# Kernel tuning notes

Measured on AMD Instinct MI355X. Metric: run time of the kernel, lower is better.

## Reference

```python
import jax, jax.numpy as jnp
import numpy as np

B, H, W, C = 32, 56, 56, 192
WS, SHIFT, HEADS = 7, 3, 6
HEAD_DIM = C // HEADS
SCALE = 0.17677669529663687  # 1/sqrt(32), passed as qk_scale
HIDDEN = 4 * C
N = WS * WS
EPS = 1e-3


def _rel_index(ws):
    coords = np.stack(np.meshgrid(np.arange(ws), np.arange(ws), indexing='ij')).reshape(2, -1)
    rel = (coords[:, :, None] - coords[:, None, :]).transpose(1, 2, 0)
    rel[:, :, 0] += ws - 1
    rel[:, :, 1] += ws - 1
    rel[:, :, 0] *= 2 * ws - 1
    return rel.sum(-1)  # [N, N] int


def _attn_mask(h, w, ws, ss):
    img = np.zeros((h, w), np.float32)
    cnt = 0
    for hs in (slice(0, -ws), slice(-ws, -ss), slice(-ss, None)):
        for wsl in (slice(0, -ws), slice(-ws, -ss), slice(-ss, None)):
            img[hs, wsl] = cnt
            cnt += 1
    win = img.reshape(h // ws, ws, w // ws, ws).transpose(0, 2, 1, 3).reshape(-1, ws * ws)
    diff = win[:, None, :] - win[:, :, None]
    return np.where(diff != 0, -100.0, 0.0).astype(np.float32)  # [nW, N, N]


REL_IDX = jnp.asarray(_rel_index(WS).reshape(-1))          # [N*N]
ATTN_MASK = jnp.asarray(_attn_mask(H, W, WS, SHIFT))       # [nW, N, N]
NW = ATTN_MASK.shape[0]


def _window_partition(x, ws):
    b, h, w, c = x.shape
    x = x.reshape(b, h // ws, ws, w // ws, ws, c).transpose(0, 1, 3, 2, 4, 5)
    return x.reshape(-1, ws, ws, c)


def _window_reverse(x, ws, h, w):
    c = x.shape[-1]
    x = x.reshape(-1, h // ws, w // ws, ws, ws, c).transpose(0, 1, 3, 2, 4, 5)
    return x.reshape(-1, h, w, c)


def _layer_norm(x, g, b):
    mu = jnp.mean(x, axis=-1, keepdims=True)
    var = jnp.var(x, axis=-1, keepdims=True)
    return (x - mu) * jax.lax.rsqrt(var + EPS) * g + b


def _forward(x, ln1_g, ln1_b, w_qkv, b_qkv, bias_table, w_proj, b_proj,
             ln2_g, ln2_b, w_ffn1, bn1_scale, bn1_shift, w_ffn2, bn2_scale, bn2_shift):
    shortcut = x
    h = _layer_norm(x, ln1_g, ln1_b)
    h = jnp.roll(h, (-SHIFT, -SHIFT), axis=(1, 2))
    xw = _window_partition(h, WS).reshape(-1, N, C)  # [B*nW, N, C]

    qkv = xw @ w_qkv + b_qkv                          # [B*nW, N, 3C]
    qkv = qkv.reshape(-1, N, 3, HEADS, HEAD_DIM).transpose(2, 0, 3, 1, 4)
    q, k, v = qkv[0] * SCALE, qkv[1], qkv[2]          # [B*nW, heads, N, hd]

    attn = jnp.einsum('whnd,whmd->whnm', q, k)        # [B*nW, heads, N, N]
    rel_bias = bias_table[REL_IDX].reshape(N, N, HEADS).transpose(2, 0, 1)
    attn = attn + rel_bias[None]
    attn = attn.reshape(-1, NW, HEADS, N, N) + ATTN_MASK[None, :, None]
    attn = jax.nn.softmax(attn.reshape(-1, HEADS, N, N), axis=-1)

    o = jnp.einsum('whnm,whmd->whnd', attn, v)        # [B*nW, heads, N, hd]
    o = o.transpose(0, 2, 1, 3).reshape(-1, N, C)
    o = o @ w_proj + b_proj

    o = _window_reverse(o.reshape(-1, WS, WS, C), WS, H, W)
    o = jnp.roll(o, (SHIFT, SHIFT), axis=(1, 2))
    x = shortcut + o

    y = _layer_norm(x, ln2_g, ln2_b)
    dn = ('NHWC', 'HWIO', 'NHWC')
    y = jax.lax.conv_general_dilated(y, w_ffn1, (1, 1), 'SAME', dimension_numbers=dn)
    y = y * bn1_scale + bn1_shift
    y = jax.nn.gelu(y, approximate=False)
    y = jax.lax.conv_general_dilated(y, w_ffn2, (1, 1), 'SAME', dimension_numbers=dn)
    y = y * bn2_scale + bn2_shift
    return x + y


def setup_inputs() -> dict:
    key = jax.random.key(0)
    ks = jax.random.split(key, 8)
    s = lambda n: 0.02
    return {
        'x': jax.random.normal(ks[0], (B, H, W, C), jnp.float32),
        'ln1_g': jnp.ones((C,), jnp.float32),
        'ln1_b': jnp.zeros((C,), jnp.float32),
        'w_qkv': jax.random.normal(ks[1], (C, 3 * C), jnp.float32) * (C ** -0.5),
        'b_qkv': jnp.zeros((3 * C,), jnp.float32),
        'bias_table': jax.random.truncated_normal(ks[2], -2.0, 2.0, ((2 * WS - 1) ** 2, HEADS), jnp.float32) * 0.02,
        'w_proj': jax.random.normal(ks[3], (C, C), jnp.float32) * (C ** -0.5),
        'b_proj': jnp.zeros((C,), jnp.float32),
        'ln2_g': jnp.ones((C,), jnp.float32),
        'ln2_b': jnp.zeros((C,), jnp.float32),
        'w_ffn1': jax.random.normal(ks[4], (3, 3, C, HIDDEN), jnp.float32) * ((9 * C) ** -0.5),
        'bn1_scale': jnp.ones((HIDDEN,), jnp.float32),
        'bn1_shift': jnp.zeros((HIDDEN,), jnp.float32),
        'w_ffn2': jax.random.normal(ks[5], (1, 1, HIDDEN, C), jnp.float32) * (HIDDEN ** -0.5),
        'bn2_scale': jnp.ones((C,), jnp.float32),
        'bn2_shift': jnp.zeros((C,), jnp.float32),
    }


def reference(x, ln1_g, ln1_b, w_qkv, b_qkv, bias_table, w_proj, b_proj,
              ln2_g, ln2_b, w_ffn1, bn1_scale, bn1_shift, w_ffn2, bn2_scale, bn2_shift):
    return _forward(x, ln1_g, ln1_b, w_qkv, b_qkv, bias_table, w_proj, b_proj,
                    ln2_g, ln2_b, w_ffn1, bn1_scale, bn1_shift, w_ffn2, bn2_scale, bn2_shift)
```

## Files before the change

### kernel.cpp

```cpp
#include <hip/hip_runtime.h>
#include <hip/hip_bf16.h>
#include <math.h>

#define DEVINL __device__ __forceinline__

typedef __bf16 bf16x8 __attribute__((ext_vector_type(8)));
typedef float  f32x4  __attribute__((ext_vector_type(4)));
typedef unsigned int u32x4 __attribute__((ext_vector_type(4)));

DEVINL float bf2f(unsigned short h){ return __builtin_bit_cast(float, (unsigned)h << 16); }
DEVINL unsigned short f2bf(float f){
  unsigned u = __builtin_bit_cast(unsigned, f);
  u += 0x7fffu + ((u >> 16) & 1u);
  return (unsigned short)(u >> 16);
}

DEVINL void gl16(const unsigned short* g, unsigned short* l){
  __builtin_amdgcn_global_load_lds((const __attribute__((address_space(1))) unsigned int*)g,
                                   (__attribute__((address_space(3))) unsigned int*)l,
                                   16, 0, 0);
}

DEVINL unsigned ldsoff(const void* p){
  return (unsigned)(unsigned long long)(const __attribute__((address_space(3))) char*)p;
}
DEVINL bf16x8 dsr16(const unsigned short* p){
  u32x4 r;
  asm volatile("ds_read_b128 %0, %1" : "=v"(r) : "v"(ldsoff(p)));
  return __builtin_bit_cast(bf16x8, r);
}

#define Bn 32
#define Hn 56
#define Wn 56
#define Cn 192
#define WSz 7
#define SHIFTn 3
#define HEADSn 6
#define HDn 32
#define NWIN 49
#define NPIX (Bn*Hn*Wn)
#define HIDDENn 768
#define KCONV (9*Cn)
#define PADH 58
#define QKSCALE 0.17677669529663687f

DEVINL float wave_sum(float v){
  #pragma unroll
  for (int off=32; off; off>>=1) v += __shfl_xor(v, off, 64);
  return v;
}

__global__ __launch_bounds__(256) void k_ln1(const float* __restrict__ x,
                                             const float* __restrict__ g,
                                             const float* __restrict__ bb,
                                             unsigned short* __restrict__ h)
{
  int row  = blockIdx.x*4 + (threadIdx.x >> 6);
  int lane = threadIdx.x & 63;
  int win = row / NWIN, n = row % NWIN;
  int b = win >> 6, rem = win & 63, wh = rem >> 3, ww = rem & 7;
  int i = n / WSz, j = n % WSz;
  int rr = (wh*WSz + i + SHIFTn) % Hn;
  int cc = (ww*WSz + j + SHIFTn) % Wn;
  const float* xr = x + (size_t)((b*Hn + rr)*Wn + cc)*Cn;
  float v0 = xr[lane], v1 = xr[lane+64], v2 = xr[lane+128];
  float s  = wave_sum(v0+v1+v2);
  float sq = wave_sum(v0*v0+v1*v1+v2*v2);
  float mu = s * (1.0f/Cn);
  float var = sq * (1.0f/Cn) - mu*mu;
  float rs = rsqrtf(var + 1e-3f);
  unsigned short* hr = h + (size_t)row*Cn;
  hr[lane]     = f2bf((v0-mu)*rs*g[lane]     + bb[lane]);
  hr[lane+64]  = f2bf((v1-mu)*rs*g[lane+64]  + bb[lane+64]);
  hr[lane+128] = f2bf((v2-mu)*rs*g[lane+128] + bb[lane+128]);
}

__global__ __launch_bounds__(256) void k_ln2(const float* __restrict__ xmid,
                                             const float* __restrict__ g,
                                             const float* __restrict__ bb,
                                             unsigned short* __restrict__ out)
{
  int p    = blockIdx.x*4 + (threadIdx.x >> 6);
  int lane = threadIdx.x & 63;
  int b = p / (Hn*Wn), rc = p % (Hn*Wn);
  int r = rc / Wn, c = rc % Wn;
  const float* xr = xmid + (size_t)p*Cn;
  float v0 = xr[lane], v1 = xr[lane+64], v2 = xr[lane+128];
  float s  = wave_sum(v0+v1+v2);
  float sq = wave_sum(v0*v0+v1*v1+v2*v2);
  float mu = s * (1.0f/Cn);
  float var = sq * (1.0f/Cn) - mu*mu;
  float rs = rsqrtf(var + 1e-3f);
  unsigned short* orow = out + (size_t)((b*PADH + r + 1)*PADH + (c + 1))*Cn;
  orow[lane]     = f2bf((v0-mu)*rs*g[lane]     + bb[lane]);
  orow[lane+64]  = f2bf((v1-mu)*rs*g[lane+64]  + bb[lane+64]);
  orow[lane+128] = f2bf((v2-mu)*rs*g[lane+128] + bb[lane+128]);
}

__global__ __launch_bounds__(256) void k_transpose(const float* __restrict__ in,
                                                   unsigned short* __restrict__ out,
                                                   int K, int N)
{
  int idx = blockIdx.x*256 + threadIdx.x;
  if (idx < K*N){ int k = idx / N, n = idx - k*N; out[(size_t)n*K + k] = f2bf(in[idx]); }
}

__global__ __launch_bounds__(256) void k_attn(const unsigned short* __restrict__ qkv,
                                              const float* __restrict__ bias_table,
                                              unsigned short* __restrict__ o,
                                              int win_base)
{
  __shared__ float qs[NWIN][HDn], ks[NWIN][HDn], vs[NWIN][HDn], S[NWIN][NWIN+1];
  int head = blockIdx.x, lwin = blockIdx.y;
  int gwin = win_base + lwin;
  int tid = threadIdx.x;
  const unsigned short* base = qkv + (size_t)lwin*NWIN*576 + head*HDn;
  for (int t = tid; t < NWIN*HDn; t += 256){
    int n = t >> 5, d = t & 31;
    const unsigned short* rp = base + (size_t)n*576 + d;
    qs[n][d] = bf2f(rp[0]) * QKSCALE;
    ks[n][d] = bf2f(rp[192]);
    vs[n][d] = bf2f(rp[384]);
  }
  __syncthreads();
  int rem = gwin & 63, wh = rem >> 3, ww = rem & 7;
  for (int t = tid; t < NWIN*NWIN; t += 256){
    int p = t / NWIN, q = t - p*NWIN;
    float acc = 0.f;
    #pragma unroll
    for (int d = 0; d < HDn; ++d) acc += qs[p][d]*ks[q][d];
    int pi = p/7, pj = p%7, qi = q/7, qj = q%7;
    int rel = (pi-qi+6)*13 + (pj-qj+6);
    acc += bias_table[rel*HEADSn + head];
    int pr = wh*7+pi, pc = ww*7+pj, qr = wh*7+qi, qc = ww*7+qj;
    int cp = (pr<49?0:(pr<53?1:2))*3 + (pc<49?0:(pc<53?1:2));
    int cq = (qr<49?0:(qr<53?1:2))*3 + (qc<49?0:(qc<53?1:2));
    if (cp != cq) acc -= 100.0f;
    S[p][q] = acc;
  }
  __syncthreads();
  if (tid < NWIN){
    float m = -1e30f;
    for (int q=0;q<NWIN;++q) m = fmaxf(m, S[tid][q]);
    float sum = 0.f;
    for (int q=0;q<NWIN;++q){ float e = expf(S[tid][q]-m); S[tid][q]=e; sum+=e; }
    float inv = 1.0f/sum;
    for (int q=0;q<NWIN;++q) S[tid][q] *= inv;
  }
  __syncthreads();
  for (int t = tid; t < NWIN*HDn; t += 256){
    int n = t >> 5, d = t & 31;
    float acc = 0.f;
    for (int m=0;m<NWIN;++m) acc += S[n][m]*vs[m][d];
    o[((size_t)gwin*NWIN + n)*Cn + head*HDn + d] = f2bf(acc);
  }
}

template<int AMODE, int EPI, int BMt, int BNt>
__global__ __launch_bounds__(256) void k_gemm(const unsigned short* __restrict__ A,
                                              const unsigned short* __restrict__ Bt,
                                              int K, int a_rbase, int o_rbase,
                                              const float* __restrict__ e0,
                                              const float* __restrict__ e1,
                                              const float* __restrict__ e2,
                                              void* __restrict__ out)
{
  constexpr int WMT = BMt/32, WNT = BNt/32;
  constexpr int NIA = BMt/64, NIB = BNt/64;
  __shared__ __align__(16) unsigned short As[BMt*32];
  __shared__ __align__(16) unsigned short Bs[BNt*32];
  int tid = threadIdx.x;
  int bm = blockIdx.y * BMt, bn = blockIdx.x * BNt;
  int wave = tid >> 6, lane = tid & 63;
  int l15 = lane & 15, quad = lane >> 4;
  int wm = (wave & 1) * (BMt/2), wn = (wave >> 1) * (BNt/2);

  int srow = tid >> 2;
  int kc   = (tid & 3) * 8;

  size_t abase[NIA];
  #pragma unroll
  for (int i=0;i<NIA;++i){
    int lrow = bm + i*64 + srow;
    if (AMODE == 0) abase[i] = (size_t)(a_rbase + lrow) * K + kc;
    else {
      int grow = a_rbase + lrow;
      int b = grow / (Hn*Wn), rc = grow % (Hn*Wn);
      int r = rc / Wn, c = rc - r*Wn;
      abase[i] = (size_t)((b*PADH + r)*PADH + c) * Cn + kc;
    }
  }
  size_t bbase[NIB];
  #pragma unroll
  for (int i=0;i<NIB;++i) bbase[i] = (size_t)(bn + i*64 + srow) * K + kc;

  f32x4 acc[WMT][WNT] = {};

  int nkb = K / 32;
  for (int kb = 0; kb < nkb; ++kb){
    int k0 = kb * 32;
    size_t aoff;
    if (AMODE == 0) aoff = (size_t)k0;
    else {
      int tap = k0 / Cn, ci = k0 - tap*Cn;
      int dh = tap/3, dw = tap - dh*3;
      aoff = (size_t)((dh*PADH + dw)*Cn + ci);
    }
    #pragma unroll
    for (int i=0;i<NIA;++i)
      gl16(A + abase[i] + aoff, &As[i*64*32] + (size_t)tid*8);
    #pragma unroll
    for (int i=0;i<NIB;++i)
      gl16(Bt + bbase[i] + (size_t)k0, &Bs[i*64*32] + (size_t)tid*8);
    __syncthreads();

    bf16x8 af[WMT], bfr[WNT];
    #pragma unroll
    for (int mt=0;mt<WMT;++mt) af[mt]  = *(const bf16x8*)&As[(wm + mt*16 + l15)*32 + quad*8];
    #pragma unroll
    for (int nt=0;nt<WNT;++nt) bfr[nt] = *(const bf16x8*)&Bs[(wn + nt*16 + l15)*32 + quad*8];
    #pragma unroll
    for (int mt=0;mt<WMT;++mt)
      #pragma unroll
      for (int nt=0;nt<WNT;++nt)
        acc[mt][nt] = __builtin_amdgcn_mfma_f32_16x16x32_bf16(af[mt], bfr[nt], acc[mt][nt], 0,0,0);
    __syncthreads();
  }

  #pragma unroll
  for (int mt=0; mt<WMT; ++mt)
  #pragma unroll
  for (int nt=0; nt<WNT; ++nt){
    f32x4 a4 = acc[mt][nt];
    int gcol = bn + wn + nt*16 + l15;
    #pragma unroll
    for (int r=0; r<4; ++r){
      int orow = bm + wm + mt*16 + quad*4 + r;
      float v = a4[r];
      if (EPI == 0){
        v += e0[gcol];
        ((unsigned short*)out)[(size_t)orow*576 + gcol] = f2bf(v);
      } else if (EPI == 1){
        v += e0[gcol];
        int grow = o_rbase + orow;
        int win = grow / NWIN, n = grow - win*NWIN;
        int b = win >> 6, rem2 = win & 63, wh = rem2 >> 3, ww = rem2 & 7;
        int ii = n / WSz, jj = n - ii*WSz;
        int fr = (wh*WSz + ii + SHIFTn) % Hn;
        int fc = (ww*WSz + jj + SHIFTn) % Wn;
        size_t idx = (size_t)((b*Hn + fr)*Wn + fc)*Cn + gcol;
        ((float*)out)[idx] = e2[idx] + v;
      } else if (EPI == 2){
        v = v * e0[gcol] + e1[gcol];
        v = 0.5f * v * (1.0f + erff(v * 0.7071067811865476f));
        ((unsigned short*)out)[(size_t)orow*HIDDENn + gcol] = f2bf(v);
      } else {
        v = v * e0[gcol] + e1[gcol];
        int grow = o_rbase + orow;
        v += e2[(size_t)grow*Cn + gcol];
        ((float*)out)[(size_t)grow*Cn + gcol] = v;
      }
    }
  }
}

__global__ __launch_bounds__(512, 1) void k_gemm8conv(
    const unsigned short* __restrict__ A,
    const unsigned short* __restrict__ Bt,
    int a_rbase,
    const float* __restrict__ e0,
    const float* __restrict__ e1,
    unsigned short* __restrict__ out)
{
  __shared__ __align__(16) unsigned short As[2*256*64];
  __shared__ __align__(16) unsigned short Bs[2*256*64];
  const int tid  = threadIdx.x;
  const int wave = tid >> 6, lane = tid & 63;
  const int l15  = lane & 15, quad = lane >> 4;
  const int wm   = (wave & 1) * 128;
  const int wn   = (wave >> 1) * 64;

  const int nwg = gridDim.x * gridDim.y;
  const int lin = blockIdx.y * gridDim.x + blockIdx.x;
  const int q8 = nwg >> 3, r8 = nwg & 7;
  const int xcd = lin & 7, cidx = lin >> 3;
  const int swz = (xcd < r8 ? xcd*(q8+1) : r8*(q8+1) + (xcd - r8)*q8) + cidx;
  const int bn = (swz % gridDim.x) * 256;
  const int bm = (swz / gridDim.x) * 256;

  const int srow = tid >> 3;
  const int scs  = (tid & 7) ^ (srow & 7);
  const int ldst = tid * 8;

  size_t abase[4], bbase[4];
  #pragma unroll
  for (int i=0;i<4;++i){
    int grow = a_rbase + bm + i*64 + srow;
    int b = grow / (Hn*Wn), rc = grow % (Hn*Wn);
    int r = rc / Wn, c = rc - r*Wn;
    abase[i] = (size_t)((b*PADH + r)*PADH + c)*Cn + scs*8;
    bbase[i] = (size_t)(bn + i*64 + srow)*KCONV + scs*8;
  }

  const int cx0 = ((quad    ) ^ (l15 & 7)) * 8;
  const int cx1 = ((quad + 4) ^ (l15 & 7)) * 8;

  f32x4 acc[8][4] = {};
  bf16x8 af[4][2], bfr[4][2];

  const int ntot = KCONV/64;

  #pragma unroll
  for (int i=0;i<4;++i) gl16(Bt + bbase[i],      Bs + i*4096 + ldst);
  #pragma unroll
  for (int i=0;i<4;++i) gl16(A  + abase[i],      As + i*4096 + ldst);
  #pragma unroll
  for (int i=0;i<4;++i) gl16(Bt + bbase[i] + 64, Bs + 16384 + i*4096 + ldst);
  #pragma unroll
  for (int i=0;i<4;++i) gl16(A  + abase[i] + 64, As + 16384 + i*4096 + ldst);
  asm volatile("s_waitcnt vmcnt(8)" ::: "memory");
  __builtin_amdgcn_s_barrier();

  for (int t = 0; t < ntot; ++t){
    const unsigned short* Ac = As + (t&1)*16384;
    const unsigned short* Bc = Bs + (t&1)*16384;
    unsigned short* Asn = As + (t&1)*16384;
    unsigned short* Bsn = Bs + (t&1)*16384;
    const bool pf = (t+2 < ntot);
    const int t2 = t + 2;
    const int tap2 = t2/3;
    const int dh2 = tap2/3, dw2 = tap2 - dh2*3, ci2 = (t2 - tap2*3)*64;
    const size_t aoff2 = (size_t)(dh2*PADH + dw2)*Cn + ci2;
    const size_t boff2 = (size_t)t2*64;

    #pragma unroll
    for (int mt=0; mt<4; ++mt){
      const unsigned short* rp = Ac + (wm + mt*16 + l15)*64;
      af[mt][0] = dsr16(rp + cx0);
      af[mt][1] = dsr16(rp + cx1);
    }
    #pragma unroll
    for (int nn=0; nn<4; ++nn){
      const unsigned short* rp = Bc + (wn + nn*16 + l15)*64;
      bfr[nn][0] = dsr16(rp + cx0);
      bfr[nn][1] = dsr16(rp + cx1);
    }
    asm volatile("s_waitcnt lgkmcnt(4)" ::: "memory");
    __builtin_amdgcn_sched_barrier(0);
    __builtin_amdgcn_s_setprio(1);
    #pragma unroll
    for (int mt=0; mt<4; ++mt)
      #pragma unroll
      for (int nn=0; nn<2; ++nn)
        #pragma unroll
        for (int kk=0; kk<2; ++kk)
          acc[mt][nn] = __builtin_amdgcn_mfma_f32_16x16x32_bf16(af[mt][kk], bfr[nn][kk], acc[mt][nn], 0,0,0);
    __builtin_amdgcn_s_setprio(0);
    asm volatile("s_waitcnt lgkmcnt(0)" ::: "memory");
    __builtin_amdgcn_sched_barrier(0);
    __builtin_amdgcn_s_setprio(1);
    #pragma unroll
    for (int mt=0; mt<4; ++mt)
      #pragma unroll
      for (int nn=2; nn<4; ++nn)
        #pragma unroll
        for (int kk=0; kk<2; ++kk)
          acc[mt][nn] = __builtin_amdgcn_mfma_f32_16x16x32_bf16(af[mt][kk], bfr[nn][kk], acc[mt][nn], 0,0,0);
    __builtin_amdgcn_s_setprio(0);
    __builtin_amdgcn_s_barrier();
    if (pf){ gl16(Bt + bbase[0] + boff2, Bsn + 0*4096 + ldst);
             gl16(Bt + bbase[1] + boff2, Bsn + 1*4096 + ldst);
             gl16(Bt + bbase[2] + boff2, Bsn + 2*4096 + ldst);
             gl16(Bt + bbase[3] + boff2, Bsn + 3*4096 + ldst); }

    #pragma unroll
    for (int mt=0; mt<4; ++mt){
      const unsigned short* rp = Ac + (wm + 64 + mt*16 + l15)*64;
      af[mt][0] = dsr16(rp + cx0);
      af[mt][1] = dsr16(rp + cx1);
    }
    asm volatile("s_waitcnt lgkmcnt(0)" ::: "memory");
    __builtin_amdgcn_sched_barrier(0);
    __builtin_amdgcn_s_setprio(1);
    #pragma unroll
    for (int mt=0; mt<4; ++mt)
      #pragma unroll
      for (int nn=0; nn<4; ++nn)
        #pragma unroll
        for (int kk=0; kk<2; ++kk)
          acc[4+mt][nn] = __builtin_amdgcn_mfma_f32_16x16x32_bf16(af[mt][kk], bfr[nn][kk], acc[4+mt][nn], 0,0,0);
    __builtin_amdgcn_s_setprio(0);
    __builtin_amdgcn_s_barrier();
    if (pf){ gl16(A + abase[0] + aoff2, Asn + 0*4096 + ldst);
             gl16(A + abase[1] + aoff2, Asn + 1*4096 + ldst);
             gl16(A + abase[2] + aoff2, Asn + 2*4096 + ldst);
             gl16(A + abase[3] + aoff2, Asn + 3*4096 + ldst); }
    if (pf)                  { asm volatile("s_waitcnt vmcnt(8)" ::: "memory"); }
    else if (t+1 < ntot)     { asm volatile("s_waitcnt vmcnt(0)" ::: "memory"); }
    __builtin_amdgcn_s_barrier();
  }

  const int orow0 = bm + wm + quad*4;
  #pragma unroll
  for (int nn=0; nn<4; ++nn){
    int gcol = bn + wn + nn*16 + l15;
    float s0 = e0[gcol], s1 = e1[gcol];
    #pragma unroll
    for (int mt=0; mt<8; ++mt){
      #pragma unroll
      for (int r=0; r<4; ++r){
        float v = acc[mt][nn][r] * s0 + s1;
        v = 0.5f * v * (1.0f + erff(v * 0.7071067811865476f));
        out[(size_t)(orow0 + mt*16 + r)*HIDDENn + gcol] = f2bf(v);
      }
    }
  }
}

extern "C" void kernel_launch(void* const* d_in, const int* in_sizes, int n_in,
                              void* d_out, int out_size, void* d_ws, size_t ws_size,
                              hipStream_t stream)
{
  const float* x        = (const float*)d_in[0];
  const float* ln1_g    = (const float*)d_in[1];
  const float* ln1_b    = (const float*)d_in[2];
  const float* w_qkv    = (const float*)d_in[3];
  const float* b_qkv    = (const float*)d_in[4];
  const float* btab     = (const float*)d_in[5];
  const float* w_proj   = (const float*)d_in[6];
  const float* b_proj   = (const float*)d_in[7];
  const float* ln2_g    = (const float*)d_in[8];
  const float* ln2_b    = (const float*)d_in[9];
  const float* w_ffn1   = (const float*)d_in[10];
  const float* bn1_s    = (const float*)d_in[11];
  const float* bn1_sh   = (const float*)d_in[12];
  const float* w_ffn2   = (const float*)d_in[13];
  const float* bn2_s    = (const float*)d_in[14];
  const float* bn2_sh   = (const float*)d_in[15];

  const size_t szA   = 41337344;
  const size_t ob_sz = (size_t)NPIX*Cn*2;
  const size_t wtsz  = 221184 + 73728 + 2654208 + 294912;
  int nch = 8;
  for (int cand = 1; cand <= 8; cand <<= 1){
    size_t qcsz  = (size_t)NPIX*1152/cand;
    size_t hcsz  = (size_t)NPIX*1536/cand;
    size_t bsz_c = qcsz + ob_sz;
    if (hcsz > bsz_c) bsz_c = hcsz;
    if (szA + bsz_c + wtsz + (1u<<20) <= ws_size){ nch = cand; break; }
  }
  const size_t qc_sz = (size_t)NPIX*1152/nch;
  size_t bsz = qc_sz + ob_sz;
  { size_t hcsz = (size_t)NPIX*1536/nch; if (hcsz > bsz) bsz = hcsz; }
  const int mc = NPIX / nch;
  const int wc = 2048 / nch;

  char* ws = (char*)d_ws;
  unsigned short* h      = (unsigned short*)ws;
  unsigned short* ln2pad = (unsigned short*)ws;
  unsigned short* qc     = (unsigned short*)(ws + szA);
  unsigned short* obuf   = (unsigned short*)(ws + szA + qc_sz);
  unsigned short* hc     = (unsigned short*)(ws + szA);
  size_t off = szA + bsz;
  unsigned short* wTq    = (unsigned short*)(ws + off);  off += 221184;
  unsigned short* wTp    = (unsigned short*)(ws + off);  off += 73728;
  unsigned short* wTf1   = (unsigned short*)(ws + off);  off += 2654208;
  unsigned short* wTf2   = (unsigned short*)(ws + off);
  float*          xmid   = (float*)d_out;
  float*          outp   = (float*)d_out;

  dim3 blk(256);

  k_transpose<<<(192*576 + 255)/256,  blk, 0, stream>>>(w_qkv,  wTq,  192, 576);
  k_transpose<<<(192*192 + 255)/256,  blk, 0, stream>>>(w_proj, wTp,  192, 192);
  k_transpose<<<(1728*768 + 255)/256, blk, 0, stream>>>(w_ffn1, wTf1, 1728, 768);
  k_transpose<<<(768*192 + 255)/256,  blk, 0, stream>>>(w_ffn2, wTf2, 768, 192);

  k_ln1<<<NPIX/4, blk, 0, stream>>>(x, ln1_g, ln1_b, h);

  for (int c = 0; c < nch; ++c){
    int rbase = c * mc;
    k_gemm<0,0,128,64><<<dim3(576/64, mc/128), blk, 0, stream>>>(
        h, wTq, 192, rbase, 0, b_qkv, nullptr, nullptr, qc);
    k_attn<<<dim3(HEADSn, wc), blk, 0, stream>>>(qc, btab, obuf, c*wc);
  }

  k_gemm<0,1,128,64><<<dim3(192/64, NPIX/128), blk, 0, stream>>>(
      obuf, wTp, 192, 0, 0, b_proj, nullptr, x, xmid);

  hipMemsetAsync(ln2pad, 0, (size_t)Bn*PADH*PADH*Cn*2, stream);
  k_ln2<<<NPIX/4, blk, 0, stream>>>(xmid, ln2_g, ln2_b, ln2pad);

  for (int c = 0; c < nch; ++c){
    int rbase = c * mc;
    k_gemm8conv<<<dim3(HIDDENn/256, mc/256), dim3(512), 0, stream>>>(
        ln2pad, wTf1, rbase, bn1_s, bn1_sh, hc);
    k_gemm<0,3,128,64><<<dim3(192/64, mc/128), blk, 0, stream>>>(
        hc, wTf2, 768, 0, rbase, bn2_s, bn2_sh, xmid, outp);
  }
}
```

Before: 1.049 ms.

## Restructure FFN1 conv GEMM mainloop into 8-phase interleaved load/MFMA pipeline

```diff
diff --git a/kernel.cpp b/kernel.cpp
--- a/kernel.cpp
+++ b/kernel.cpp
@@ -310,94 +310,212 @@
   bf16x8 af[4][2], bfr[4][2];
 
   const int ntot = KCONV/64;
-
-  #pragma unroll
-  for (int i=0;i<4;++i) gl16(Bt + bbase[i],      Bs + i*4096 + ldst);
-  #pragma unroll
-  for (int i=0;i<4;++i) gl16(A  + abase[i],      As + i*4096 + ldst);
-  #pragma unroll
-  for (int i=0;i<4;++i) gl16(Bt + bbase[i] + 64, Bs + 16384 + i*4096 + ldst);
-  #pragma unroll
-  for (int i=0;i<4;++i) gl16(A  + abase[i] + 64, As + 16384 + i*4096 + ldst);
-  asm volatile("s_waitcnt vmcnt(8)" ::: "memory");
+  const int nit  = (ntot+1)/2;
+
+  auto AOFF = [](int t)->size_t{
+    int tap = t/3, ci = (t - tap*3)*64;
+    int dh = tap/3, dw = tap - dh*3;
+    return (size_t)((dh*PADH + dw)*Cn + ci);
+  };
+
+  gl16(A  + abase[0],            As + 0*4096 + ldst);
+  gl16(A  + abase[1],            As + 1*4096 + ldst);
+  gl16(A  + abase[2],            As + 2*4096 + ldst);
+  gl16(A  + abase[3],            As + 3*4096 + ldst);
+  gl16(Bt + bbase[0],            Bs + 0*4096 + ldst);
+  gl16(Bt + bbase[1],            Bs + 1*4096 + ldst);
+  gl16(Bt + bbase[2],            Bs + 2*4096 + ldst);
+  gl16(Bt + bbase[3],            Bs + 3*4096 + ldst);
+  {
+    size_t a1 = AOFF(1);
+    gl16(A  + abase[0] + a1,      As + 16384 + 0*4096 + ldst);
+    gl16(A  + abase[2] + a1,      As + 16384 + 2*4096 + ldst);
+    gl16(Bt + bbase[0] + 64,      Bs + 16384 + 0*4096 + ldst);
+    gl16(Bt + bbase[1] + 64,      Bs + 16384 + 1*4096 + ldst);
+    gl16(Bt + bbase[2] + 64,      Bs + 16384 + 2*4096 + ldst);
+    gl16(Bt + bbase[3] + 64,      Bs + 16384 + 3*4096 + ldst);
+  }
+  asm volatile("s_waitcnt vmcnt(6)" ::: "memory");
   __builtin_amdgcn_s_barrier();
 
-  for (int t = 0; t < ntot; ++t){
-    const unsigned short* Ac = As + (t&1)*16384;
-    const unsigned short* Bc = Bs + (t&1)*16384;
-    unsigned short* Asn = As + (t&1)*16384;
-    unsigned short* Bsn = Bs + (t&1)*16384;
-    const bool pf = (t+2 < ntot);
-    const int t2 = t + 2;
-    const int tap2 = t2/3;
-    const int dh2 = tap2/3, dw2 = tap2 - dh2*3, ci2 = (t2 - tap2*3)*64;
-    const size_t aoff2 = (size_t)(dh2*PADH + dw2)*Cn + ci2;
-    const size_t boff2 = (size_t)t2*64;
+  for (int i = 0; i < nit; ++i){
+    const int e = 2*i, o = 2*i+1, e2 = e+2, o2 = o+2;
+    const size_t aoffo  = AOFF(o);
+    const size_t aoffe2 = (e2 < ntot) ? AOFF(e2) : 0;
+    const size_t aoffo2 = (o2 < ntot) ? AOFF(o2) : 0;
+    const size_t boffe2 = (size_t)e2*64, boffo2 = (size_t)o2*64;
 
     #pragma unroll
     for (int mt=0; mt<4; ++mt){
-      const unsigned short* rp = Ac + (wm + mt*16 + l15)*64;
-      af[mt][0] = dsr16(rp + cx0);
-      af[mt][1] = dsr16(rp + cx1);
-    }
-    #pragma unroll
-    for (int nn=0; nn<4; ++nn){
-      const unsigned short* rp = Bc + (wn + nn*16 + l15)*64;
-      bfr[nn][0] = dsr16(rp + cx0);
-      bfr[nn][1] = dsr16(rp + cx1);
-    }
-    asm volatile("s_waitcnt lgkmcnt(4)" ::: "memory");
-    __builtin_amdgcn_sched_barrier(0);
-    __builtin_amdgcn_s_setprio(1);
-    #pragma unroll
-    for (int mt=0; mt<4; ++mt)
-      #pragma unroll
-      for (int nn=0; nn<2; ++nn)
-        #pragma unroll
-        for (int kk=0; kk<2; ++kk)
-          acc[mt][nn] = __builtin_amdgcn_mfma_f32_16x16x32_bf16(af[mt][kk], bfr[nn][kk], acc[mt][nn], 0,0,0);
-    __builtin_amdgcn_s_setprio(0);
+      const unsigned short* rp = As + (wm + mt*16 + l15)*64;
+      af[mt][0] = dsr16(rp + cx0);  af[mt][1] = dsr16(rp + cx1);
+    }
+    #pragma unroll
+    for (int nn=0; nn<2; ++nn){
+      const unsigned short* rp = Bs + (wn + nn*16 + l15)*64;
+      bfr[nn][0] = dsr16(rp + cx0); bfr[nn][1] = dsr16(rp + cx1);
+    }
+    if (o < ntot){ gl16(A + abase[1] + aoffo, As + 16384 + 1*4096 + ldst);
+                   gl16(A + abase[3] + aoffo, As + 16384 + 3*4096 + ldst); }
+    asm volatile("s_waitcnt lgkmcnt(8)" ::: "memory");
+    __builtin_amdgcn_s_barrier();
     asm volatile("s_waitcnt lgkmcnt(0)" ::: "memory");
     __builtin_amdgcn_sched_barrier(0);
     __builtin_amdgcn_s_setprio(1);
     #pragma unroll
     for (int mt=0; mt<4; ++mt)
       #pragma unroll
-      for (int nn=2; nn<4; ++nn)
+      for (int nn=0; nn<2; ++nn)
         #pragma unroll
         for (int kk=0; kk<2; ++kk)
           acc[mt][nn] = __builtin_amdgcn_mfma_f32_16x16x32_bf16(af[mt][kk], bfr[nn][kk], acc[mt][nn], 0,0,0);
     __builtin_amdgcn_s_setprio(0);
     __builtin_amdgcn_s_barrier();
-    if (pf){ gl16(Bt + bbase[0] + boff2, Bsn + 0*4096 + ldst);
-             gl16(Bt + bbase[1] + boff2, Bsn + 1*4096 + ldst);
-             gl16(Bt + bbase[2] + boff2, Bsn + 2*4096 + ldst);
-             gl16(Bt + bbase[3] + boff2, Bsn + 3*4096 + ldst); }
-
-    #pragma unroll
-    for (int mt=0; mt<4; ++mt){
-      const unsigned short* rp = Ac + (wm + 64 + mt*16 + l15)*64;
-      af[mt][0] = dsr16(rp + cx0);
-      af[mt][1] = dsr16(rp + cx1);
-    }
+
+    #pragma unroll
+    for (int nn=2; nn<4; ++nn){
+      const unsigned short* rp = Bs + (wn + nn*16 + l15)*64;
+      bfr[nn][0] = dsr16(rp + cx0); bfr[nn][1] = dsr16(rp + cx1);
+    }
+    if (e2 < ntot){ gl16(A + abase[0] + aoffe2, As + 0*4096 + ldst);
+                    gl16(A + abase[2] + aoffe2, As + 2*4096 + ldst); }
+    __builtin_amdgcn_s_barrier();
     asm volatile("s_waitcnt lgkmcnt(0)" ::: "memory");
     __builtin_amdgcn_sched_barrier(0);
     __builtin_amdgcn_s_setprio(1);
     #pragma unroll
     for (int mt=0; mt<4; ++mt)
       #pragma unroll
-      for (int nn=0; nn<4; ++nn)
+      for (int nn=2; nn<4; ++nn)
+        #pragma unroll
+        for (int kk=0; kk<2; ++kk)
+          acc[mt][nn] = __builtin_amdgcn_mfma_f32_16x16x32_bf16(af[mt][kk], bfr[nn][kk], acc[mt][nn], 0,0,0);
+    __builtin_amdgcn_s_setprio(0);
+    __builtin_amdgcn_s_barrier();
+
+    #pragma unroll
+    for (int mt=0; mt<4; ++mt){
+      const unsigned short* rp = As + (wm + 64 + mt*16 + l15)*64;
+      af[mt][0] = dsr16(rp + cx0);  af[mt][1] = dsr16(rp + cx1);
+    }
+    if (e2 < ntot){ gl16(Bt + bbase[0] + boffe2, Bs + 0*4096 + ldst);
+                    gl16(Bt + bbase[1] + boffe2, Bs + 1*4096 + ldst); }
+    __builtin_amdgcn_s_barrier();
+    asm volatile("s_waitcnt lgkmcnt(0)" ::: "memory");
+    __builtin_amdgcn_sched_barrier(0);
+    __builtin_amdgcn_s_setprio(1);
+    #pragma unroll
+    for (int mt=0; mt<4; ++mt)
+      #pragma unroll
+      for (int nn=0; nn<2; ++nn)
         #pragma unroll
         for (int kk=0; kk<2; ++kk)
           acc[4+mt][nn] = __builtin_amdgcn_mfma_f32_16x16x32_bf16(af[mt][kk], bfr[nn][kk], acc[4+mt][nn], 0,0,0);
     __builtin_amdgcn_s_setprio(0);
     __builtin_amdgcn_s_barrier();
-    if (pf){ gl16(A + abase[0] + aoff2, Asn + 0*4096 + ldst);
-             gl16(A + abase[1] + aoff2, Asn + 1*4096 + ldst);
-             gl16(A + abase[2] + aoff2, Asn + 2*4096 + ldst);
-             gl16(A + abase[3] + aoff2, Asn + 3*4096 + ldst); }
-    if (pf)                  { asm volatile("s_waitcnt vmcnt(8)" ::: "memory"); }
-    else if (t+1 < ntot)     { asm volatile("s_waitcnt vmcnt(0)" ::: "memory"); }
+
+    if (e2 < ntot){ gl16(Bt + bbase[2] + boffe2, Bs + 2*4096 + ldst);
+                    gl16(Bt + bbase[3] + boffe2, Bs + 3*4096 + ldst); }
+    __builtin_amdgcn_s_setprio(1);
+    #pragma unroll
+    for (int mt=0; mt<4; ++mt)
+      #pragma unroll
+      for (int nn=2; nn<4; ++nn)
+        #pragma unroll
+        for (int kk=0; kk<2; ++kk)
+          acc[4+mt][nn] = __builtin_amdgcn_mfma_f32_16x16x32_bf16(af[mt][kk], bfr[nn][kk], acc[4+mt][nn], 0,0,0);
+    __builtin_amdgcn_s_setprio(0);
+    if (e2 < ntot) { asm volatile("s_waitcnt vmcnt(6)" ::: "memory"); }
+    else           { asm volatile("s_waitcnt vmcnt(0)" ::: "memory"); }
+    __builtin_amdgcn_s_barrier();
+
+    if (o >= ntot) break;
+
+    const unsigned short* A1c = As + 16384;
+    const unsigned short* B1c = Bs + 16384;
+
+    #pragma unroll
+    for (int mt=0; mt<4; ++mt){
+      const unsigned short* rp = A1c + (wm + mt*16 + l15)*64;
+      af[mt][0] = dsr16(rp + cx0);  af[mt][1] = dsr16(rp + cx1);
+    }
+    #pragma unroll
+    for (int nn=0; nn<2; ++nn){
+      const unsigned short* rp = B1c + (wn + nn*16 + l15)*64;
+      bfr[nn][0] = dsr16(rp + cx0); bfr[nn][1] = dsr16(rp + cx1);
+    }
+    if (e2 < ntot){ gl16(A + abase[1] + aoffe2, As + 1*4096 + ldst);
+                    gl16(A + abase[3] + aoffe2, As + 3*4096 + ldst); }
+    asm volatile("s_waitcnt lgkmcnt(8)" ::: "memory");
+    __builtin_amdgcn_s_barrier();
+    asm volatile("s_waitcnt lgkmcnt(0)" ::: "memory");
+    __builtin_amdgcn_sched_barrier(0);
+    __builtin_amdgcn_s_setprio(1);
+    #pragma unroll
+    for (int mt=0; mt<4; ++mt)
+      #pragma unroll
+      for (int nn=0; nn<2; ++nn)
+        #pragma unroll
+        for (int kk=0; kk<2; ++kk)
+          acc[mt][nn] = __builtin_amdgcn_mfma_f32_16x16x32_bf16(af[mt][kk], bfr[nn][kk], acc[mt][nn], 0,0,0);
+    __builtin_amdgcn_s_setprio(0);
+    __builtin_amdgcn_s_barrier();
+
+    #pragma unroll
+    for (int nn=2; nn<4; ++nn){
+      const unsigned short* rp = B1c + (wn + nn*16 + l15)*64;
+      bfr[nn][0] = dsr16(rp + cx0); bfr[nn][1] = dsr16(rp + cx1);
+    }
+    if (o2 < ntot){ gl16(A + abase[0] + aoffo2, As + 16384 + 0*4096 + ldst);
+                    gl16(A + abase[2] + aoffo2, As + 16384 + 2*4096 + ldst); }
+    __builtin_amdgcn_s_barrier();
+    asm volatile("s_waitcnt lgkmcnt(0)" ::: "memory");
+    __builtin_amdgcn_sched_barrier(0);
+    __builtin_amdgcn_s_setprio(1);
+    #pragma unroll
+    for (int mt=0; mt<4; ++mt)
+      #pragma unroll
+      for (int nn=2; nn<4; ++nn)
+        #pragma unroll
+        for (int kk=0; kk<2; ++kk)
+          acc[mt][nn] = __builtin_amdgcn_mfma_f32_16x16x32_bf16(af[mt][kk], bfr[nn][kk], acc[mt][nn], 0,0,0);
+    __builtin_amdgcn_s_setprio(0);
+    __builtin_amdgcn_s_barrier();
+
+    #pragma unroll
+    for (int mt=0; mt<4; ++mt){
+      const unsigned short* rp = A1c + (wm + 64 + mt*16 + l15)*64;
+      af[mt][0] = dsr16(rp + cx0);  af[mt][1] = dsr16(rp + cx1);
+    }
+    if (o2 < ntot){ gl16(Bt + bbase[0] + boffo2, Bs + 16384 + 0*4096 + ldst);
+                    gl16(Bt + bbase[1] + boffo2, Bs + 16384 + 1*4096 + ldst); }
+    __builtin_amdgcn_s_barrier();
+    asm volatile("s_waitcnt lgkmcnt(0)" ::: "memory");
+    __builtin_amdgcn_sched_barrier(0);
+    __builtin_amdgcn_s_setprio(1);
+    #pragma unroll
+    for (int mt=0; mt<4; ++mt)
+      #pragma unroll
+      for (int nn=0; nn<2; ++nn)
+        #pragma unroll
+        for (int kk=0; kk<2; ++kk)
+          acc[4+mt][nn] = __builtin_amdgcn_mfma_f32_16x16x32_bf16(af[mt][kk], bfr[nn][kk], acc[4+mt][nn], 0,0,0);
+    __builtin_amdgcn_s_setprio(0);
+    __builtin_amdgcn_s_barrier();
+
+    if (o2 < ntot){ gl16(Bt + bbase[2] + boffo2, Bs + 16384 + 2*4096 + ldst);
+                    gl16(Bt + bbase[3] + boffo2, Bs + 16384 + 3*4096 + ldst); }
+    __builtin_amdgcn_s_setprio(1);
+    #pragma unroll
+    for (int mt=0; mt<4; ++mt)
+      #pragma unroll
+      for (int nn=2; nn<4; ++nn)
+        #pragma unroll
+        for (int kk=0; kk<2; ++kk)
+          acc[4+mt][nn] = __builtin_amdgcn_mfma_f32_16x16x32_bf16(af[mt][kk], bfr[nn][kk], acc[4+mt][nn], 0,0,0);
+    __builtin_amdgcn_s_setprio(0);
+    if (o2 < ntot) { asm volatile("s_waitcnt vmcnt(6)" ::: "memory"); }
+    else           { asm volatile("s_waitcnt vmcnt(0)" ::: "memory"); }
     __builtin_amdgcn_s_barrier();
   }
 
```

New measurement: 1.753 ms. 67.1% more time.
